# Kernel tuning notes

Measured on AMD Instinct MI355X. Metric: run time of the kernel, lower is better.

Reference implementation:

```python
import jax, jax.numpy as jnp
import numpy as np

GH, GW = 64, 64     # patch grid
WH, WW = 8, 8       # window size
NH = 8              # num heads
EMB = 128
HD = EMB // NH      # head dim = 16
M = WH * WW         # tokens per window = 64


def _masks():
    # Faithful to the torch code: row_mask blocks cross-shift attention for the
    # last window-row; column_mask is its einops-rearranged counterpart.
    half = WH * (WW // 2)
    row = np.zeros((M, M), np.float32)
    row[-half:, :-half] = -np.inf
    row[:-half, -half:] = -np.inf
    r, c = M // WH, M // WW
    # '(r wh) (c ww) -> (wh r) (ww c)'
    col = row.reshape(r, WH, c, WW).transpose(1, 0, 3, 2).reshape(M, M)
    return jnp.asarray(row), jnp.asarray(col)


def _rel_idx():
    hh, ww_ = np.meshgrid(np.arange(WH), np.arange(WW), indexing='ij')
    coords = np.stack([hh.ravel(), ww_.ravel()], -1)        # (M, 2)
    rel = coords[:, None, :] - coords[None, :, :]           # (M, M, 2)
    return jnp.asarray(rel[..., 0] + WH - 1), jnp.asarray(rel[..., 1] + WW - 1)


def setup_inputs() -> dict:
    key = jax.random.key(0)
    ks = jax.random.split(key, 4)
    B, L = 32, GH * GW
    return {
        'x': jax.random.normal(ks[0], (B, L, EMB), jnp.float32),
        'w1': jax.random.normal(ks[1], (3 * EMB, EMB), jnp.float32) * 0.02,
        'b1': jnp.zeros((3 * EMB,), jnp.float32),
        'w2': jax.random.normal(ks[2], (EMB, EMB), jnp.float32) * 0.02,
        'b2': jnp.zeros((EMB,), jnp.float32),
        'rel_bias': jax.random.normal(ks[3], (2 * WH - 1, 2 * WW - 1), jnp.float32) * 0.02,
    }


def reference(x, w1, b1, w2, b2, rel_bias):
    B, L, C = x.shape
    qkv = x @ w1.T + b1                                   # (B, L, 3C)
    # 'b (h w) (c k) -> b h w c k'  (k=3 varies fastest within channel)
    qkv = qkv.reshape(B, GH, GW, C, 3)
    # cyclic shift by half window
    qkv = jnp.roll(qkv, (-WH // 2, -WW // 2), axis=(1, 2))
    # 'b (Hw wh) (Ww ww) (e H) k -> b H Hw Ww (wh ww) e k'  (head idx fastest in C)
    qkv = qkv.reshape(B, GH // WH, WH, GW // WW, WW, HD, NH, 3)
    qkv = jnp.transpose(qkv, (0, 6, 1, 3, 2, 4, 5, 7))    # b H Hw Ww wh ww e k
    qkv = qkv.reshape(B, NH, GH // WH, GW // WW, M, HD, 3)
    Q, K, V = qkv[..., 0], qkv[..., 1], qkv[..., 2]
    wei = jnp.einsum('bhijqe,bhijke->bhijqk', Q, K) / float(np.sqrt(HD))
    ih, iw = _rel_idx()
    wei = wei + rel_bias[ih, iw]                          # (M, M) bias broadcast
    row_mask, col_mask = _masks()
    wei = wei.at[:, :, -1, :].add(row_mask)               # last window-row
    wei = wei.at[:, :, :, -1].add(col_mask)               # last window-col
    attn = jax.nn.softmax(wei, axis=-1)
    out = jnp.einsum('bhijqk,bhijke->bhijqe', attn, V)    # b H Hw Ww M e
    # 'b H Hw Ww (wh ww) e -> b (Hw wh) (Ww ww) (H e)' then flatten spatial
    out = out.reshape(B, NH, GH // WH, GW // WW, WH, WW, HD)
    out = jnp.transpose(out, (0, 2, 4, 3, 5, 1, 6)).reshape(B, L, C)
    return out @ w2.T + b2
```

## Files before the change

kernel.cpp:

```cpp
#include <hip/hip_runtime.h>
#include <math.h>

typedef _Float16 h4  __attribute__((ext_vector_type(4)));
typedef _Float16 h8  __attribute__((ext_vector_type(8)));
typedef __fp16   g2  __attribute__((ext_vector_type(2)));
typedef float    f4  __attribute__((ext_vector_type(4)));
typedef float    f32x4 __attribute__((ext_vector_type(4)));

#define W1_ELEMS (384*128)
#define W2_ELEMS (128*128)
#define BM_ELEMS (4*64*64)
#define LOG2E 1.44269504088896340736f

static __device__ __forceinline__ h4 pk4(float a, float b, float c, float d) {
    union { struct { g2 l, h; } g; h4 v; } u;
    u.g.l = __builtin_amdgcn_cvt_pkrtz(a, b);
    u.g.h = __builtin_amdgcn_cvt_pkrtz(c, d);
    return u.v;
}

__global__ void cvt_weights(const float* __restrict__ w1, const float* __restrict__ w2,
                            const float* __restrict__ rel_bias,
                            _Float16* __restrict__ w1h, _Float16* __restrict__ w2h,
                            _Float16* __restrict__ bmg) {
    int i = blockIdx.x * 256 + threadIdx.x;
    if (i < W1_ELEMS) {
        int j = i >> 7, k = i & 127;
        int c = j / 3;
        int kind = j - 3 * c;
        int jp = kind * 128 + (c & 7) * 16 + (c >> 3);
        float v = w1[i];
        if (kind == 0) v *= 0.25f * LOG2E;
        w1h[jp * 128 + k] = (_Float16)v;
    }
    if (i < W2_ELEMS) w2h[i] = (_Float16)w2[i];
    if (i < BM_ELEMS) {
        int v = i >> 12, e = i & 4095;
        int lane = (e >> 2) & 63;
        int ti = ((e >> 10) & 3) * 16 + (lane & 15);
        int tj = ((e >> 8) & 3) * 16 + (lane >> 4) * 4 + (e & 3);
        float val = rel_bias[((ti >> 3) - (tj >> 3) + 7) * 15 + ((ti & 7) - (tj & 7) + 7)] * LOG2E;
        if ((v & 2) && ((ti ^ tj) & 32)) val = -INFINITY;
        if ((v & 1) && ((ti ^ tj) & 4))  val = -INFINITY;
        bmg[i] = (_Float16)val;
    }
}

__global__ __launch_bounds__(512, 4)
void swin_fused(const float* __restrict__ x,
                const float* __restrict__ b1,
                const float* __restrict__ b2,
                const _Float16* __restrict__ w1h,
                const _Float16* __restrict__ w2h,
                const _Float16* __restrict__ bmg,
                float* __restrict__ out)
{
    __shared__ _Float16 xh[64*136];
    __shared__ _Float16 Ob[64*136];
    __shared__ float    bmf[4096];

    const int tid  = threadIdx.x;
    const int lane = tid & 63;
    const int wv   = tid >> 6;
    const int quad = lane >> 4;
    const int l16  = lane & 15;

    const int blk = blockIdx.x;
    const int b   = blk >> 6;
    const int Hw  = (blk >> 3) & 7;
    const int Ww  = blk & 7;

    {
        const int variant = (((Hw == 7) ? 2 : 0) | ((Ww == 7) ? 1 : 0));
        h8 v = *(const h8*)(bmg + (variant << 12) + tid*8);
        f32x4 lo = { (float)v[0], (float)v[1], (float)v[2], (float)v[3] };
        f32x4 hi = { (float)v[4], (float)v[5], (float)v[6], (float)v[7] };
        *(f32x4*)(&bmf[tid*8])     = lo;
        *(f32x4*)(&bmf[tid*8 + 4]) = hi;
    }
    {
        const int r0 = tid >> 5;
        const int c4 = tid & 31;
        #pragma unroll
        for (int it = 0; it < 4; ++it) {
            int t  = r0 + it*16;
            int gi = (Hw*8 + (t >> 3) + 4) & 63;
            int gj = (Ww*8 + (t & 7) + 4) & 63;
            f32x4 v = *(const f32x4*)(x + ((size_t)b*4096 + gi*64 + gj)*128 + c4*4);
            *(h4*)(&xh[t*136 + c4*4]) = pk4(v[0], v[1], v[2], v[3]);
        }
    }

    const float qsc = 0.25f * LOG2E;
    f4 cQ, cK;
    #pragma unroll
    for (int r = 0; r < 4; ++r) {
        cQ[r] = b1[24*(quad*4 + r) + 3*wv + 0] * qsc;
        cK[r] = b1[24*(quad*4 + r) + 3*wv + 1];
    }
    const float bV = b1[24*l16 + 3*wv + 2];
    const f4 cV = {bV, bV, bV, bV};

    __syncthreads();

    h4 qb[4], ak[4], av[4];
    {
        f4 accQ[4], accK[4];
        #pragma unroll
        for (int tt = 0; tt < 4; ++tt) { accQ[tt] = cQ; accK[tt] = cK; }
        for (int kb = 0; kb < 4; ++kb) {
            h8 bfx[4];
            #pragma unroll
            for (int tt = 0; tt < 4; ++tt)
                bfx[tt] = *(const h8*)(&xh[(tt*16 + l16)*136 + kb*32 + quad*8]);
            h8 aQ = *(const h8*)(w1h + (size_t)((0*8 + wv)*16 + l16)*128 + kb*32 + quad*8);
            h8 aK = *(const h8*)(w1h + (size_t)((1*8 + wv)*16 + l16)*128 + kb*32 + quad*8);
            #pragma unroll
            for (int tt = 0; tt < 4; ++tt) {
                accQ[tt] = __builtin_amdgcn_mfma_f32_16x16x32_f16(aQ, bfx[tt], accQ[tt], 0, 0, 0);
                accK[tt] = __builtin_amdgcn_mfma_f32_16x16x32_f16(aK, bfx[tt], accK[tt], 0, 0, 0);
            }
        }
        #pragma unroll
        for (int mt = 0; mt < 4; ++mt) {
            qb[mt] = pk4(accQ[mt][0], accQ[mt][1], accQ[mt][2], accQ[mt][3]);
            ak[mt] = pk4(accK[mt][0], accK[mt][1], accK[mt][2], accK[mt][3]);
        }
    }
    {
        f4 accV[4];
        #pragma unroll
        for (int tt = 0; tt < 4; ++tt) accV[tt] = cV;
        for (int kb = 0; kb < 4; ++kb) {
            h8 bfx[4];
            #pragma unroll
            for (int tt = 0; tt < 4; ++tt)
                bfx[tt] = *(const h8*)(&xh[(tt*16 + l16)*136 + kb*32 + quad*8]);
            h8 aV = *(const h8*)(w1h + (size_t)((2*8 + wv)*16 + l16)*128 + kb*32 + quad*8);
            #pragma unroll
            for (int tt = 0; tt < 4; ++tt)
                accV[tt] = __builtin_amdgcn_mfma_f32_16x16x32_f16(bfx[tt], aV, accV[tt], 0, 0, 0);
        }
        #pragma unroll
        for (int kt = 0; kt < 4; ++kt)
            av[kt] = pk4(accV[kt][0], accV[kt][1], accV[kt][2], accV[kt][3]);
    }

    for (int nt = 0; nt < 4; ++nt) {
        f4 T[4];
        #pragma unroll
        for (int mt = 0; mt < 4; ++mt) {
            f4 c = *(const f4*)(&bmf[((nt*4 + mt)*64 + lane)*4]);
            T[mt] = __builtin_amdgcn_mfma_f32_16x16x16f16(ak[mt], qb[nt], c, 0, 0, 0);
        }
        float p[16];
        #pragma unroll
        for (int mt = 0; mt < 4; ++mt)
            #pragma unroll
            for (int r = 0; r < 4; ++r)
                p[mt*4 + r] = __builtin_amdgcn_exp2f(T[mt][r]);
        float s = ((p[0]+p[1]) + (p[2]+p[3])) + ((p[4]+p[5]) + (p[6]+p[7]))
                + ((p[8]+p[9]) + (p[10]+p[11])) + ((p[12]+p[13]) + (p[14]+p[15]));
        s += __shfl_xor(s, 16, 64);
        s += __shfl_xor(s, 32, 64);
        float rcp = 1.0f / s;

        h4 P[4];
        #pragma unroll
        for (int mt = 0; mt < 4; ++mt)
            P[mt] = pk4(p[mt*4], p[mt*4+1], p[mt*4+2], p[mt*4+3]);

        f4 o = {0.f,0.f,0.f,0.f};
        #pragma unroll
        for (int kt = 0; kt < 4; ++kt)
            o = __builtin_amdgcn_mfma_f32_16x16x16f16(av[kt], P[kt], o, 0, 0, 0);
        h4 ov = pk4(o[0]*rcp, o[1]*rcp, o[2]*rcp, o[3]*rcp);
        *(h4*)(&Ob[(nt*16 + l16)*136 + wv*16 + quad*4]) = ov;
    }
    __syncthreads();

    {
        const int o = wv*16 + l16;
        const float b2o = b2[o];
        const f4 cO = {b2o, b2o, b2o, b2o};

        f4 acc3[4];
        #pragma unroll
        for (int mt = 0; mt < 4; ++mt) acc3[mt] = cO;
        for (int kb = 0; kb < 4; ++kb) {
            h8 bf = *(const h8*)(w2h + (size_t)o*128 + kb*32 + quad*8);
            #pragma unroll
            for (int mt = 0; mt < 4; ++mt) {
                h8 af = *(const h8*)(&Ob[(mt*16 + l16)*136 + kb*32 + quad*8]);
                acc3[mt] = __builtin_amdgcn_mfma_f32_16x16x32_f16(af, bf, acc3[mt], 0, 0, 0);
            }
        }
        #pragma unroll
        for (int mt = 0; mt < 4; ++mt) {
            #pragma unroll
            for (int r = 0; r < 4; ++r) {
                int t  = mt*16 + quad*4 + r;
                int gi = Hw*8 + (t >> 3);
                int gj = Ww*8 + (t & 7);
                out[((size_t)b*4096 + gi*64 + gj)*128 + o] = acc3[mt][r];
            }
        }
    }
}

extern "C" void kernel_launch(void* const* d_in, const int* in_sizes, int n_in,
                              void* d_out, int out_size, void* d_ws, size_t ws_size,
                              hipStream_t stream) {
    (void)in_sizes; (void)n_in; (void)out_size; (void)ws_size;
    const float* x  = (const float*)d_in[0];
    const float* w1 = (const float*)d_in[1];
    const float* b1 = (const float*)d_in[2];
    const float* w2 = (const float*)d_in[3];
    const float* b2 = (const float*)d_in[4];
    const float* rb = (const float*)d_in[5];

    _Float16* w1h = (_Float16*)d_ws;
    _Float16* w2h = (_Float16*)((char*)d_ws + (size_t)W1_ELEMS * sizeof(_Float16));
    _Float16* bmg = (_Float16*)((char*)d_ws + (size_t)(W1_ELEMS + W2_ELEMS) * sizeof(_Float16));
    float* outp = (float*)d_out;

    cvt_weights<<<(W1_ELEMS + 255)/256, 256, 0, stream>>>(w1, w2, rb, w1h, w2h, bmg);
    swin_fused<<<32*64, 512, 0, stream>>>(x, b1, b2, w1h, w2h, bmg, outp);
}
```

Measured before the change: 148.4 us.

## Process four windows per block with register-prefetched next-window input

Each block now handles four consecutive windows in a row instead of one, so the grid drops from 2048 to 512 blocks. The bias/mask table is loaded once per block and reloaded only for the last column window. The next window's x tile is loaded into registers during attention compute and written to shared memory after a barrier, overlapping global loads with MFMA work. The risk is reduced parallelism (512 blocks of 512 threads on a large GPU) and extra barriers per window.

Result: slower. 201.9 us (+36.0%).

```diff
diff --git a/kernel.cpp b/kernel.cpp
--- a/kernel.cpp
+++ b/kernel.cpp
@@ -65,31 +65,15 @@
     const int quad = lane >> 4;
     const int l16  = lane & 15;
 
-    const int blk = blockIdx.x;
-    const int b   = blk >> 6;
-    const int Hw  = (blk >> 3) & 7;
-    const int Ww  = blk & 7;
-
-    {
-        const int variant = (((Hw == 7) ? 2 : 0) | ((Ww == 7) ? 1 : 0));
-        h8 v = *(const h8*)(bmg + (variant << 12) + tid*8);
-        f32x4 lo = { (float)v[0], (float)v[1], (float)v[2], (float)v[3] };
-        f32x4 hi = { (float)v[4], (float)v[5], (float)v[6], (float)v[7] };
-        *(f32x4*)(&bmf[tid*8])     = lo;
-        *(f32x4*)(&bmf[tid*8 + 4]) = hi;
-    }
-    {
-        const int r0 = tid >> 5;
-        const int c4 = tid & 31;
-        #pragma unroll
-        for (int it = 0; it < 4; ++it) {
-            int t  = r0 + it*16;
-            int gi = (Hw*8 + (t >> 3) + 4) & 63;
-            int gj = (Ww*8 + (t & 7) + 4) & 63;
-            f32x4 v = *(const f32x4*)(x + ((size_t)b*4096 + gi*64 + gj)*128 + c4*4);
-            *(h4*)(&xh[t*136 + c4*4]) = pk4(v[0], v[1], v[2], v[3]);
-        }
-    }
+    const int blk  = blockIdx.x;
+    const int b    = blk >> 4;
+    const int rem  = blk & 15;
+    const int Hw   = rem >> 1;
+    const int Wq   = (rem & 1) * 4;
+    const int rowm = (Hw == 7) ? 2 : 0;
+
+    const int r0 = tid >> 5;
+    const int c4 = tid & 31;
 
     const float qsc = 0.25f * LOG2E;
     f4 cQ, cK;
@@ -101,110 +85,160 @@
     const float bV = b1[24*l16 + 3*wv + 2];
     const f4 cV = {bV, bV, bV, bV};
 
+    {
+        h8 v = *(const h8*)(bmg + (rowm << 12) + tid*8);
+        f32x4 lo = { (float)v[0], (float)v[1], (float)v[2], (float)v[3] };
+        f32x4 hi = { (float)v[4], (float)v[5], (float)v[6], (float)v[7] };
+        *(f32x4*)(&bmf[tid*8])     = lo;
+        *(f32x4*)(&bmf[tid*8 + 4]) = hi;
+    }
+    f32x4 xr[4];
+    #pragma unroll
+    for (int it = 0; it < 4; ++it) {
+        int t  = r0 + it*16;
+        int gi = (Hw*8 + (t >> 3) + 4) & 63;
+        int gj = (Wq*8 + (t & 7) + 4) & 63;
+        xr[it] = *(const f32x4*)(x + ((size_t)b*4096 + gi*64 + gj)*128 + c4*4);
+    }
+    #pragma unroll
+    for (int it = 0; it < 4; ++it) {
+        int t = r0 + it*16;
+        *(h4*)(&xh[t*136 + c4*4]) = pk4(xr[it][0], xr[it][1], xr[it][2], xr[it][3]);
+    }
     __syncthreads();
 
-    h4 qb[4], ak[4], av[4];
-    {
-        f4 accQ[4], accK[4];
-        #pragma unroll
-        for (int tt = 0; tt < 4; ++tt) { accQ[tt] = cQ; accK[tt] = cK; }
-        for (int kb = 0; kb < 4; ++kb) {
-            h8 bfx[4];
-            #pragma unroll
-            for (int tt = 0; tt < 4; ++tt)
-                bfx[tt] = *(const h8*)(&xh[(tt*16 + l16)*136 + kb*32 + quad*8]);
-            h8 aQ = *(const h8*)(w1h + (size_t)((0*8 + wv)*16 + l16)*128 + kb*32 + quad*8);
-            h8 aK = *(const h8*)(w1h + (size_t)((1*8 + wv)*16 + l16)*128 + kb*32 + quad*8);
-            #pragma unroll
-            for (int tt = 0; tt < 4; ++tt) {
-                accQ[tt] = __builtin_amdgcn_mfma_f32_16x16x32_f16(aQ, bfx[tt], accQ[tt], 0, 0, 0);
-                accK[tt] = __builtin_amdgcn_mfma_f32_16x16x32_f16(aK, bfx[tt], accK[tt], 0, 0, 0);
-            }
-        }
-        #pragma unroll
-        for (int mt = 0; mt < 4; ++mt) {
-            qb[mt] = pk4(accQ[mt][0], accQ[mt][1], accQ[mt][2], accQ[mt][3]);
-            ak[mt] = pk4(accK[mt][0], accK[mt][1], accK[mt][2], accK[mt][3]);
-        }
-    }
-    {
-        f4 accV[4];
-        #pragma unroll
-        for (int tt = 0; tt < 4; ++tt) accV[tt] = cV;
-        for (int kb = 0; kb < 4; ++kb) {
-            h8 bfx[4];
-            #pragma unroll
-            for (int tt = 0; tt < 4; ++tt)
-                bfx[tt] = *(const h8*)(&xh[(tt*16 + l16)*136 + kb*32 + quad*8]);
-            h8 aV = *(const h8*)(w1h + (size_t)((2*8 + wv)*16 + l16)*128 + kb*32 + quad*8);
-            #pragma unroll
-            for (int tt = 0; tt < 4; ++tt)
-                accV[tt] = __builtin_amdgcn_mfma_f32_16x16x32_f16(bfx[tt], aV, accV[tt], 0, 0, 0);
-        }
-        #pragma unroll
-        for (int kt = 0; kt < 4; ++kt)
-            av[kt] = pk4(accV[kt][0], accV[kt][1], accV[kt][2], accV[kt][3]);
-    }
-
-    for (int nt = 0; nt < 4; ++nt) {
-        f4 T[4];
-        #pragma unroll
-        for (int mt = 0; mt < 4; ++mt) {
-            f4 c = *(const f4*)(&bmf[((nt*4 + mt)*64 + lane)*4]);
-            T[mt] = __builtin_amdgcn_mfma_f32_16x16x16f16(ak[mt], qb[nt], c, 0, 0, 0);
-        }
-        float p[16];
-        #pragma unroll
-        for (int mt = 0; mt < 4; ++mt)
-            #pragma unroll
-            for (int r = 0; r < 4; ++r)
-                p[mt*4 + r] = __builtin_amdgcn_exp2f(T[mt][r]);
-        float s = ((p[0]+p[1]) + (p[2]+p[3])) + ((p[4]+p[5]) + (p[6]+p[7]))
-                + ((p[8]+p[9]) + (p[10]+p[11])) + ((p[12]+p[13]) + (p[14]+p[15]));
-        s += __shfl_xor(s, 16, 64);
-        s += __shfl_xor(s, 32, 64);
-        float rcp = 1.0f / s;
-
-        h4 P[4];
-        #pragma unroll
-        for (int mt = 0; mt < 4; ++mt)
-            P[mt] = pk4(p[mt*4], p[mt*4+1], p[mt*4+2], p[mt*4+3]);
-
-        f4 o = {0.f,0.f,0.f,0.f};
-        #pragma unroll
-        for (int kt = 0; kt < 4; ++kt)
-            o = __builtin_amdgcn_mfma_f32_16x16x16f16(av[kt], P[kt], o, 0, 0, 0);
-        h4 ov = pk4(o[0]*rcp, o[1]*rcp, o[2]*rcp, o[3]*rcp);
-        *(h4*)(&Ob[(nt*16 + l16)*136 + wv*16 + quad*4]) = ov;
-    }
-    __syncthreads();
-
-    {
-        const int o = wv*16 + l16;
-        const float b2o = b2[o];
-        const f4 cO = {b2o, b2o, b2o, b2o};
-
-        f4 acc3[4];
-        #pragma unroll
-        for (int mt = 0; mt < 4; ++mt) acc3[mt] = cO;
-        for (int kb = 0; kb < 4; ++kb) {
-            h8 bf = *(const h8*)(w2h + (size_t)o*128 + kb*32 + quad*8);
+    for (int w = 0; w < 4; ++w) {
+        const int Ww = Wq + w;
+
+        h4 qb[4], ak[4], av[4];
+        {
+            f4 accQ[4], accK[4];
+            #pragma unroll
+            for (int tt = 0; tt < 4; ++tt) { accQ[tt] = cQ; accK[tt] = cK; }
+            for (int kb = 0; kb < 4; ++kb) {
+                h8 bfx[4];
+                #pragma unroll
+                for (int tt = 0; tt < 4; ++tt)
+                    bfx[tt] = *(const h8*)(&xh[(tt*16 + l16)*136 + kb*32 + quad*8]);
+                h8 aQ = *(const h8*)(w1h + (size_t)((0*8 + wv)*16 + l16)*128 + kb*32 + quad*8);
+                h8 aK = *(const h8*)(w1h + (size_t)((1*8 + wv)*16 + l16)*128 + kb*32 + quad*8);
+                #pragma unroll
+                for (int tt = 0; tt < 4; ++tt) {
+                    accQ[tt] = __builtin_amdgcn_mfma_f32_16x16x32_f16(aQ, bfx[tt], accQ[tt], 0, 0, 0);
+                    accK[tt] = __builtin_amdgcn_mfma_f32_16x16x32_f16(aK, bfx[tt], accK[tt], 0, 0, 0);
+                }
+            }
             #pragma unroll
             for (int mt = 0; mt < 4; ++mt) {
-                h8 af = *(const h8*)(&Ob[(mt*16 + l16)*136 + kb*32 + quad*8]);
-                acc3[mt] = __builtin_amdgcn_mfma_f32_16x16x32_f16(af, bf, acc3[mt], 0, 0, 0);
-            }
-        }
-        #pragma unroll
-        for (int mt = 0; mt < 4; ++mt) {
-            #pragma unroll
-            for (int r = 0; r < 4; ++r) {
-                int t  = mt*16 + quad*4 + r;
-                int gi = Hw*8 + (t >> 3);
-                int gj = Ww*8 + (t & 7);
-                out[((size_t)b*4096 + gi*64 + gj)*128 + o] = acc3[mt][r];
-            }
-        }
+                qb[mt] = pk4(accQ[mt][0], accQ[mt][1], accQ[mt][2], accQ[mt][3]);
+                ak[mt] = pk4(accK[mt][0], accK[mt][1], accK[mt][2], accK[mt][3]);
+            }
+        }
+        {
+            f4 accV[4];
+            #pragma unroll
+            for (int tt = 0; tt < 4; ++tt) accV[tt] = cV;
+            for (int kb = 0; kb < 4; ++kb) {
+                h8 bfx[4];
+                #pragma unroll
+                for (int tt = 0; tt < 4; ++tt)
+                    bfx[tt] = *(const h8*)(&xh[(tt*16 + l16)*136 + kb*32 + quad*8]);
+                h8 aV = *(const h8*)(w1h + (size_t)((2*8 + wv)*16 + l16)*128 + kb*32 + quad*8);
+                #pragma unroll
+                for (int tt = 0; tt < 4; ++tt)
+                    accV[tt] = __builtin_amdgcn_mfma_f32_16x16x32_f16(bfx[tt], aV, accV[tt], 0, 0, 0);
+            }
+            #pragma unroll
+            for (int kt = 0; kt < 4; ++kt)
+                av[kt] = pk4(accV[kt][0], accV[kt][1], accV[kt][2], accV[kt][3]);
+        }
+
+        if (w < 3) {
+            #pragma unroll
+            for (int it = 0; it < 4; ++it) {
+                int t  = r0 + it*16;
+                int gi = (Hw*8 + (t >> 3) + 4) & 63;
+                int gj = ((Ww + 1)*8 + (t & 7) + 4) & 63;
+                xr[it] = *(const f32x4*)(x + ((size_t)b*4096 + gi*64 + gj)*128 + c4*4);
+            }
+        }
+
+        for (int nt = 0; nt < 4; ++nt) {
+            f4 T[4];
+            #pragma unroll
+            for (int mt = 0; mt < 4; ++mt) {
+                f4 c = *(const f4*)(&bmf[((nt*4 + mt)*64 + lane)*4]);
+                T[mt] = __builtin_amdgcn_mfma_f32_16x16x16f16(ak[mt], qb[nt], c, 0, 0, 0);
+            }
+            float p[16];
+            #pragma unroll
+            for (int mt = 0; mt < 4; ++mt)
+                #pragma unroll
+                for (int r = 0; r < 4; ++r)
+                    p[mt*4 + r] = __builtin_amdgcn_exp2f(T[mt][r]);
+            float s = ((p[0]+p[1]) + (p[2]+p[3])) + ((p[4]+p[5]) + (p[6]+p[7]))
+                    + ((p[8]+p[9]) + (p[10]+p[11])) + ((p[12]+p[13]) + (p[14]+p[15]));
+            s += __shfl_xor(s, 16, 64);
+            s += __shfl_xor(s, 32, 64);
+            float rcp = 1.0f / s;
+
+            h4 P[4];
+            #pragma unroll
+            for (int mt = 0; mt < 4; ++mt)
+                P[mt] = pk4(p[mt*4], p[mt*4+1], p[mt*4+2], p[mt*4+3]);
+
+            f4 o = {0.f,0.f,0.f,0.f};
+            #pragma unroll
+            for (int kt = 0; kt < 4; ++kt)
+                o = __builtin_amdgcn_mfma_f32_16x16x16f16(av[kt], P[kt], o, 0, 0, 0);
+            h4 ov = pk4(o[0]*rcp, o[1]*rcp, o[2]*rcp, o[3]*rcp);
+            *(h4*)(&Ob[(nt*16 + l16)*136 + wv*16 + quad*4]) = ov;
+        }
+        __syncthreads();
+
+        if (w < 3) {
+            #pragma unroll
+            for (int it = 0; it < 4; ++it) {
+                int t = r0 + it*16;
+                *(h4*)(&xh[t*136 + c4*4]) = pk4(xr[it][0], xr[it][1], xr[it][2], xr[it][3]);
+            }
+            if (w == 2 && Wq == 4) {
+                h8 v = *(const h8*)(bmg + ((rowm | 1) << 12) + tid*8);
+                f32x4 lo = { (float)v[0], (float)v[1], (float)v[2], (float)v[3] };
+                f32x4 hi = { (float)v[4], (float)v[5], (float)v[6], (float)v[7] };
+                *(f32x4*)(&bmf[tid*8])     = lo;
+                *(f32x4*)(&bmf[tid*8 + 4]) = hi;
+            }
+        }
+
+        {
+            const int o = wv*16 + l16;
+            const float b2o = b2[o];
+            const f4 cO = {b2o, b2o, b2o, b2o};
+
+            f4 acc3[4];
+            #pragma unroll
+            for (int mt = 0; mt < 4; ++mt) acc3[mt] = cO;
+            for (int kb = 0; kb < 4; ++kb) {
+                h8 bf = *(const h8*)(w2h + (size_t)o*128 + kb*32 + quad*8);
+                #pragma unroll
+                for (int mt = 0; mt < 4; ++mt) {
+                    h8 af = *(const h8*)(&Ob[(mt*16 + l16)*136 + kb*32 + quad*8]);
+                    acc3[mt] = __builtin_amdgcn_mfma_f32_16x16x32_f16(af, bf, acc3[mt], 0, 0, 0);
+                }
+            }
+            #pragma unroll
+            for (int mt = 0; mt < 4; ++mt) {
+                #pragma unroll
+                for (int r = 0; r < 4; ++r) {
+                    int t  = mt*16 + quad*4 + r;
+                    int gi = Hw*8 + (t >> 3);
+                    int gj = Ww*8 + (t & 7);
+                    out[((size_t)b*4096 + gi*64 + gj)*128 + o] = acc3[mt][r];
+                }
+            }
+        }
+        if (w < 3) __syncthreads();
     }
 }
 
@@ -225,5 +259,5 @@
     float* outp = (float*)d_out;
 
     cvt_weights<<<(W1_ELEMS + 255)/256, 256, 0, stream>>>(w1, w2, rb, w1h, w2h, bmg);
-    swin_fused<<<32*64, 512, 0, stream>>>(x, b1, b2, w1h, w2h, bmg, outp);
-}
+    swin_fused<<<512, 512, 0, stream>>>(x, b1, b2, w1h, w2h, bmg, outp);
+}
```
